# Optimization experiments

Measured on AMD Instinct MI355X. Metric: run time of the kernel, lower is better.

## Reference

```python
import jax, jax.numpy as jnp
import numpy as np

_Q_IN = 128          # Q7 fixed-point scale
_LUT_MIN = -1024     # covers exp(x) for x in [-8, 0]
_Q_OUT = 1 << 16     # Q16 output scale for exp LUT
_TOP_K = 2

# exp LUT: index i in [-1024, 0] -> int32(exp(i/128) * 2^16), matching _build_exp_lut
_EXP_LUT = (jnp.exp(jnp.arange(_LUT_MIN, 1, dtype=jnp.float32) / _Q_IN) * _Q_OUT).astype(jnp.int32)


def softmax_integer(logits):
    """Fixed-point INT32 softmax via Q16 exp LUT (drop-in for softmax)."""
    li = jnp.round(logits.astype(jnp.float32) * _Q_IN).astype(jnp.int32)
    shifted = jnp.clip(li - li.max(axis=-1, keepdims=True), _LUT_MIN, None)  # <= 0
    exp_vals = _EXP_LUT[shifted - _LUT_MIN]                                  # Q16 int32
    exp_sum = jnp.clip(exp_vals.sum(axis=-1, keepdims=True), 1, None)
    return exp_vals.astype(jnp.float32) / exp_sum.astype(jnp.float32)


def setup_inputs() -> dict:
    key = jax.random.key(0)
    k0, k1, k2, k3, k4 = jax.random.split(key, 5)
    B, S, H, I, E = 4, 2048, 2048, 5632, 8
    x = jax.random.normal(k0, (B, S, H), dtype=jnp.float32)
    w_gate = jax.random.normal(k1, (E, H), dtype=jnp.float32) * 0.02
    w1 = jax.random.normal(k2, (E, I, H), dtype=jnp.float32) * 0.02  # gate proj, [out,in]
    w2 = jax.random.normal(k3, (E, H, I), dtype=jnp.float32) * 0.02  # down proj
    w3 = jax.random.normal(k4, (E, I, H), dtype=jnp.float32) * 0.02  # up proj
    return {"x": x, "w_gate": w_gate, "w1": w1, "w2": w2, "w3": w3}


def reference(x, w_gate, w1, w2, w3):
    orig_shape = x.shape
    H = orig_shape[-1]
    xf = x.reshape(-1, H)                 # [T, H]
    T = xf.shape[0]
    E = w_gate.shape[0]

    router_logits = xf @ w_gate.T         # [T, E]
    routing_weights = softmax_integer(router_logits)
    top_w, top_i = jax.lax.top_k(routing_weights, _TOP_K)
    top_w = top_w / top_w.sum(axis=-1, keepdims=True)

    # dense per-(token, expert) combine weights; zero for unselected experts
    combine = jnp.zeros((T, E), xf.dtype).at[jnp.arange(T)[:, None], top_i].add(top_w)

    out = jnp.zeros_like(xf)
    for e in range(E):  # small fixed expert count
        h = jax.nn.silu(xf @ w1[e].T) * (xf @ w3[e].T)   # [T, I] SwiGLU
        out = out + combine[:, e:e + 1] * (h @ w2[e].T)  # weighted combine
    return out.reshape(orig_shape)
```

## Files before the change

kernel.cpp:

```cpp
#include <hip/hip_runtime.h>
#include <hip/hip_bf16.h>

#define T_TOK 8192
#define HD 2048
#define ID 5632
#define NE 8

typedef __bf16 bf16x8 __attribute__((ext_vector_type(8)));
typedef float f32x4 __attribute__((ext_vector_type(4)));

__global__ void k_build_lut(int* __restrict__ lut) {
    int i = blockIdx.x * blockDim.x + threadIdx.x;
    if (i <= 1024) {
        float xv = (float)(i - 1024) * (1.0f / 128.0f);
        lut[i] = (int)(expf(xv) * 65536.0f);
    }
}

__global__ __launch_bounds__(64)
void k_router(const float* __restrict__ x, const float* __restrict__ wg,
              const int* __restrict__ lut, int* __restrict__ counts,
              int* __restrict__ lists, float* __restrict__ wlist) {
    const int tok  = blockIdx.x;
    const int lane = threadIdx.x;
    const float* xr = x + (size_t)tok * HD;

    double dot[NE];
    #pragma unroll
    for (int e = 0; e < NE; ++e) {
        const float* wr = wg + e * HD;
        double acc = 0.0;
        for (int k = lane; k < HD; k += 64)
            acc += (double)xr[k] * (double)wr[k];
        #pragma unroll
        for (int off = 32; off > 0; off >>= 1)
            acc += __shfl_down(acc, off);
        dot[e] = acc;
    }
    if (lane == 0) {
        int li[NE];
        #pragma unroll
        for (int e = 0; e < NE; ++e)
            li[e] = (int)rintf((float)dot[e] * 128.0f);
        int m = li[0];
        #pragma unroll
        for (int e = 1; e < NE; ++e) m = li[e] > m ? li[e] : m;
        int ev[NE]; int s = 0;
        #pragma unroll
        for (int e = 0; e < NE; ++e) {
            int sh = li[e] - m;
            if (sh < -1024) sh = -1024;
            ev[e] = lut[sh + 1024];
            s += ev[e];
        }
        int i0 = 0;
        #pragma unroll
        for (int e = 1; e < NE; ++e) if (ev[e] > ev[i0]) i0 = e;
        int i1 = -1;
        #pragma unroll
        for (int e = 0; e < NE; ++e) {
            if (e == i0) continue;
            if (i1 < 0 || ev[e] > ev[i1]) i1 = e;
        }
        float fs = (float)s;
        float r0 = (float)ev[i0] / fs;
        float r1 = (float)ev[i1] / fs;
        float ts = r0 + r1;
        float w0 = r0 / ts, w1 = r1 / ts;

        int p0 = atomicAdd(&counts[i0], 1);
        lists[i0 * T_TOK + p0] = (tok << 1);
        wlist[i0 * T_TOK + p0] = w0;
        int p1 = atomicAdd(&counts[i1], 1);
        lists[i1 * T_TOK + p1] = (tok << 1) | 1;
        wlist[i1 * T_TOK + p1] = w1;
    }
}

__global__ __launch_bounds__(256)
void k_cvt_bf16(const float* __restrict__ src, __bf16* __restrict__ dst, long n8) {
    long i = (long)blockIdx.x * blockDim.x + threadIdx.x;
    const long stride = (long)gridDim.x * blockDim.x;
    for (; i < n8; i += stride) {
        const f32x4 v0 = *reinterpret_cast<const f32x4*>(src + i * 8);
        const f32x4 v1 = *reinterpret_cast<const f32x4*>(src + i * 8 + 4);
        bf16x8 h;
        h[0] = (__bf16)v0[0]; h[1] = (__bf16)v0[1]; h[2] = (__bf16)v0[2]; h[3] = (__bf16)v0[3];
        h[4] = (__bf16)v1[0]; h[5] = (__bf16)v1[1]; h[6] = (__bf16)v1[2]; h[7] = (__bf16)v1[3];
        *reinterpret_cast<bf16x8*>(dst + i * 8) = h;
    }
}

__device__ __forceinline__ void cvt_store8(void* lds_base, int woff, const float* __restrict__ src) {
    const f32x4 v0 = *reinterpret_cast<const f32x4*>(src);
    const f32x4 v1 = *reinterpret_cast<const f32x4*>(src + 4);
    bf16x8 h;
    h[0] = (__bf16)v0[0]; h[1] = (__bf16)v0[1]; h[2] = (__bf16)v0[2]; h[3] = (__bf16)v0[3];
    h[4] = (__bf16)v1[0]; h[5] = (__bf16)v1[1]; h[6] = (__bf16)v1[2]; h[7] = (__bf16)v1[3];
    *reinterpret_cast<bf16x8*>(reinterpret_cast<char*>(lds_base) + woff) = h;
}

__device__ __forceinline__ bf16x8 lds_frag(const void* lds_base, int row, int klo) {
    int off = (row * 128 + klo) ^ ((row & 7) << 4);
    return *reinterpret_cast<const bf16x8*>(reinterpret_cast<const char*>(lds_base) + off);
}

__device__ __forceinline__ void gload16(const void* g, void* l) {
    __builtin_amdgcn_global_load_lds(
        (const __attribute__((address_space(1))) unsigned int*)g,
        (__attribute__((address_space(3))) unsigned int*)l,
        16, 0, 0);
}


__global__ __launch_bounds__(512, 2)
void k_gateup_b16(const __bf16* __restrict__ xb, const __bf16* __restrict__ w1b,
                  const __bf16* __restrict__ w3b,
                  const int* __restrict__ counts, const int* __restrict__ lists,
                  __bf16* __restrict__ hbuf) {
    const int e   = blockIdx.z;
    const int cnt = counts[e];
    const int mt  = blockIdx.y;
    if (mt * 128 >= cnt) return;
    const int nt  = blockIdx.x;

    __shared__ __align__(16) __bf16 sX [2][8192];
    __shared__ __align__(16) __bf16 sW1[2][8192];
    __shared__ __align__(16) __bf16 sW3[2][8192];

    const int t    = threadIdx.x;
    const int lane = t & 63;
    const int wave = t >> 6;
    const int wm   = (wave >> 2) * 64;
    const int wn   = (wave & 3) * 32;

    const int lrow = lane >> 3;
    const int kel  = ((lane & 7) ^ lrow) * 8;

    const __bf16* gX[2]; const __bf16* g1[2]; const __bf16* g3[2];
    int ldo[2];
    #pragma unroll
    for (int cq = 0; cq < 2; ++cq) {
        const int c   = wave + cq * 8;
        const int row = c * 8 + lrow;
        int mi  = mt * 128 + row;
        int mic = mi < cnt - 1 ? mi : cnt - 1;
        int tok = lists[e * T_TOK + mic] >> 1;
        gX[cq] = xb + (size_t)tok * HD + kel;
        const int grow = nt * 128 + row;
        g1[cq] = w1b + ((size_t)e * ID + grow) * HD + kel;
        g3[cq] = w3b + ((size_t)e * ID + grow) * HD + kel;
        ldo[cq] = c * 1024;
    }

    f32x4 accg[4][2] = {};
    f32x4 accu[4][2] = {};

#define STAGE_A(b, kt) do { \
    _Pragma("unroll") \
    for (int cq = 0; cq < 2; ++cq) { \
        gload16(gX[cq] + (kt), (char*)sX [b] + ldo[cq]); \
        gload16(g1[cq] + (kt), (char*)sW1[b] + ldo[cq]); \
        gload16(g3[cq] + (kt), (char*)sW3[b] + ldo[cq]); \
    } } while (0)

#define COMPUTE_A(b) do { \
    const __bf16* bx = sX [b]; \
    const __bf16* b1 = sW1[b]; \
    const __bf16* b3 = sW3[b]; \
    __builtin_amdgcn_s_setprio(1); \
    _Pragma("unroll") \
    for (int kk = 0; kk < 2; ++kk) { \
        const int klo = kk * 64 + ((lane >> 4) << 4); \
        bf16x8 af[4], b1f[2], b3f[2]; \
        _Pragma("unroll") \
        for (int m = 0; m < 4; ++m) \
            af[m] = lds_frag(bx, wm + m * 16 + (lane & 15), klo); \
        _Pragma("unroll") \
        for (int n = 0; n < 2; ++n) { \
            int row = wn + n * 16 + (lane & 15); \
            b1f[n] = lds_frag(b1, row, klo); \
            b3f[n] = lds_frag(b3, row, klo); \
        } \
        _Pragma("unroll") \
        for (int m = 0; m < 4; ++m) \
            _Pragma("unroll") \
            for (int n = 0; n < 2; ++n) { \
                accg[m][n] = __builtin_amdgcn_mfma_f32_16x16x32_bf16(af[m], b1f[n], accg[m][n], 0, 0, 0); \
                accu[m][n] = __builtin_amdgcn_mfma_f32_16x16x32_bf16(af[m], b3f[n], accu[m][n], 0, 0, 0); \
            } \
    } \
    __builtin_amdgcn_s_setprio(0); \
    } while (0)

    const int NT = HD / 64;
    STAGE_A(0, 0);
    for (int it = 0; it < NT - 1; ++it) {
        STAGE_A((it + 1) & 1, (it + 1) * 64);
        asm volatile("s_waitcnt vmcnt(6)" ::: "memory");
        __builtin_amdgcn_s_barrier();
        COMPUTE_A(it & 1);
        __builtin_amdgcn_s_barrier();
    }
    asm volatile("s_waitcnt vmcnt(0)" ::: "memory");
    __builtin_amdgcn_s_barrier();
    COMPUTE_A((NT - 1) & 1);

    const int col_l = lane & 15;
    const int row_l = (lane >> 4) * 4;
    #pragma unroll
    for (int m = 0; m < 4; ++m) {
        #pragma unroll
        for (int j = 0; j < 4; ++j) {
            int tl = wm + m * 16 + row_l + j;
            int mi = mt * 128 + tl;
            if (mi < cnt) {
                int slot = lists[e * T_TOK + mi];
                __bf16* hrow = hbuf + (size_t)slot * ID + nt * 128 + wn;
                #pragma unroll
                for (int n = 0; n < 2; ++n) {
                    float g = accg[m][n][j];
                    float u = accu[m][n][j];
                    float hv = (g / (1.0f + expf(-g))) * u;
                    hrow[n * 16 + col_l] = (__bf16)hv;
                }
            }
        }
    }
#undef STAGE_A
#undef COMPUTE_A
}

__global__ __launch_bounds__(512, 2)
void k_down_b16(const __bf16* __restrict__ hbuf, const __bf16* __restrict__ w2b,
                const int* __restrict__ counts, const int* __restrict__ lists,
                const float* __restrict__ wlist, float* __restrict__ out) {
    const int e   = blockIdx.z;
    const int cnt = counts[e];
    const int mt  = blockIdx.y;
    if (mt * 128 >= cnt) return;
    const int nt  = blockIdx.x;

    __shared__ __align__(16) __bf16 sH[2][8192];
    __shared__ __align__(16) __bf16 sW[2][8192];

    const int t    = threadIdx.x;
    const int lane = t & 63;
    const int wave = t >> 6;
    const int wm   = (wave >> 2) * 64;
    const int wn   = (wave & 3) * 32;

    const int lrow = lane >> 3;
    const int kel  = ((lane & 7) ^ lrow) * 8;

    const __bf16* gH[2]; const __bf16* gW[2];
    int ldo[2];
    #pragma unroll
    for (int cq = 0; cq < 2; ++cq) {
        const int c   = wave + cq * 8;
        const int row = c * 8 + lrow;
        int mi  = mt * 128 + row;
        int mic = mi < cnt - 1 ? mi : cnt - 1;
        int slot = lists[e * T_TOK + mic];
        gH[cq] = hbuf + (size_t)slot * ID + kel;
        const int grow = nt * 128 + row;
        gW[cq] = w2b + ((size_t)e * HD + grow) * ID + kel;
        ldo[cq] = c * 1024;
    }

    f32x4 acc[4][2] = {};

#define STAGE_B(b, kt) do { \
    _Pragma("unroll") \
    for (int cq = 0; cq < 2; ++cq) { \
        gload16(gH[cq] + (kt), (char*)sH[b] + ldo[cq]); \
        gload16(gW[cq] + (kt), (char*)sW[b] + ldo[cq]); \
    } } while (0)

#define COMPUTE_B(b) do { \
    const __bf16* bh = sH[b]; \
    const __bf16* bw = sW[b]; \
    __builtin_amdgcn_s_setprio(1); \
    _Pragma("unroll") \
    for (int kk = 0; kk < 2; ++kk) { \
        const int klo = kk * 64 + ((lane >> 4) << 4); \
        bf16x8 af[4], bf[2]; \
        _Pragma("unroll") \
        for (int m = 0; m < 4; ++m) \
            af[m] = lds_frag(bh, wm + m * 16 + (lane & 15), klo); \
        _Pragma("unroll") \
        for (int n = 0; n < 2; ++n) \
            bf[n] = lds_frag(bw, wn + n * 16 + (lane & 15), klo); \
        _Pragma("unroll") \
        for (int m = 0; m < 4; ++m) \
            _Pragma("unroll") \
            for (int n = 0; n < 2; ++n) \
                acc[m][n] = __builtin_amdgcn_mfma_f32_16x16x32_bf16(af[m], bf[n], acc[m][n], 0, 0, 0); \
    } \
    __builtin_amdgcn_s_setprio(0); \
    } while (0)

    const int NT = ID / 64;
    STAGE_B(0, 0);
    for (int it = 0; it < NT - 1; ++it) {
        STAGE_B((it + 1) & 1, (it + 1) * 64);
        asm volatile("s_waitcnt vmcnt(4)" ::: "memory");
        __builtin_amdgcn_s_barrier();
        COMPUTE_B(it & 1);
        __builtin_amdgcn_s_barrier();
    }
    asm volatile("s_waitcnt vmcnt(0)" ::: "memory");
    __builtin_amdgcn_s_barrier();
    COMPUTE_B((NT - 1) & 1);

    const int col_l = lane & 15;
    const int row_l = (lane >> 4) * 4;
    #pragma unroll
    for (int m = 0; m < 4; ++m) {
        #pragma unroll
        for (int j = 0; j < 4; ++j) {
            int tl = wm + m * 16 + row_l + j;
            int mi = mt * 128 + tl;
            if (mi < cnt) {
                int slot = lists[e * T_TOK + mi];
                int tok  = slot >> 1;
                float w  = wlist[e * T_TOK + mi];
                float* orow = out + (size_t)tok * HD + nt * 128 + wn;
                #pragma unroll
                for (int n = 0; n < 2; ++n)
                    atomicAdd(&orow[n * 16 + col_l], w * acc[m][n][j]);
            }
        }
    }
#undef STAGE_B
#undef COMPUTE_B
}


__global__ __launch_bounds__(256)
void k_gateup_f32(const float* __restrict__ x, const float* __restrict__ w1,
                  const float* __restrict__ w3,
                  const int* __restrict__ counts, const int* __restrict__ lists,
                  __bf16* __restrict__ hbuf) {
    const int e   = blockIdx.z;
    const int cnt = counts[e];
    const int mt  = blockIdx.y;
    if (mt * 128 >= cnt) return;
    const int nt  = blockIdx.x;

    __shared__ __align__(16) __bf16 sX [128 * 64];
    __shared__ __align__(16) __bf16 sW1[128 * 64];
    __shared__ __align__(16) __bf16 sW3[128 * 64];

    const int t    = threadIdx.x;
    const int lane = t & 63;
    const int wave = t >> 6;
    const int wm   = (wave >> 1) * 64;
    const int wn   = (wave & 1) * 64;
    const int cc = t & 7;
    const int r0 = t >> 3;

    const float* srcX[4]; const float* src1[4]; const float* src3[4];
    int woff[4];
    #pragma unroll
    for (int q = 0; q < 4; ++q) {
        int row = r0 + 32 * q;
        int mi  = mt * 128 + row;
        int mic = mi < cnt - 1 ? mi : cnt - 1;
        int slot = lists[e * T_TOK + mic];
        int tok  = slot >> 1;
        srcX[q] = x + (size_t)tok * HD + cc * 8;
        int grow = nt * 128 + row;
        src1[q] = w1 + ((size_t)e * ID + grow) * HD + cc * 8;
        src3[q] = w3 + ((size_t)e * ID + grow) * HD + cc * 8;
        woff[q] = (row * 128 + cc * 16) ^ ((row & 7) << 4);
    }

    f32x4 accg[4][4] = {};
    f32x4 accu[4][4] = {};

    for (int kt = 0; kt < HD; kt += 64) {
        __syncthreads();
        #pragma unroll
        for (int q = 0; q < 4; ++q) {
            cvt_store8(sX,  srcX[q] ? woff[q] : 0, srcX[q] + kt);
            cvt_store8(sW1, woff[q], src1[q] + kt);
            cvt_store8(sW3, woff[q], src3[q] + kt);
        }
        __syncthreads();
        #pragma unroll
        for (int kk = 0; kk < 2; ++kk) {
            const int klo = kk * 64 + ((lane >> 4) << 4);
            bf16x8 af[4], b1f[4], b3f[4];
            #pragma unroll
            for (int m = 0; m < 4; ++m)
                af[m] = lds_frag(sX, wm + m * 16 + (lane & 15), klo);
            #pragma unroll
            for (int n = 0; n < 4; ++n) {
                int row = wn + n * 16 + (lane & 15);
                b1f[n] = lds_frag(sW1, row, klo);
                b3f[n] = lds_frag(sW3, row, klo);
            }
            #pragma unroll
            for (int m = 0; m < 4; ++m)
                #pragma unroll
                for (int n = 0; n < 4; ++n) {
                    accg[m][n] = __builtin_amdgcn_mfma_f32_16x16x32_bf16(af[m], b1f[n], accg[m][n], 0, 0, 0);
                    accu[m][n] = __builtin_amdgcn_mfma_f32_16x16x32_bf16(af[m], b3f[n], accu[m][n], 0, 0, 0);
                }
        }
    }

    const int col_l = lane & 15;
    const int row_l = (lane >> 4) * 4;
    #pragma unroll
    for (int m = 0; m < 4; ++m) {
        #pragma unroll
        for (int j = 0; j < 4; ++j) {
            int tl = wm + m * 16 + row_l + j;
            int mi = mt * 128 + tl;
            if (mi < cnt) {
                int slot = lists[e * T_TOK + mi];
                __bf16* hrow = hbuf + (size_t)slot * ID + nt * 128 + wn;
                #pragma unroll
                for (int n = 0; n < 4; ++n) {
                    float g = accg[m][n][j];
                    float u = accu[m][n][j];
                    float hv = (g / (1.0f + expf(-g))) * u;
                    hrow[n * 16 + col_l] = (__bf16)hv;
                }
            }
        }
    }
}

__global__ __launch_bounds__(256)
void k_down_f32(const __bf16* __restrict__ hbuf, const float* __restrict__ w2,
                const int* __restrict__ counts, const int* __restrict__ lists,
                const float* __restrict__ wlist, float* __restrict__ out) {
    const int e   = blockIdx.z;
    const int cnt = counts[e];
    const int mt  = blockIdx.y;
    if (mt * 128 >= cnt) return;
    const int nt  = blockIdx.x;

    __shared__ __align__(16) __bf16 sH[128 * 64];
    __shared__ __align__(16) __bf16 sW[128 * 64];

    const int t    = threadIdx.x;
    const int lane = t & 63;
    const int wave = t >> 6;
    const int wm   = (wave >> 1) * 64;
    const int wn   = (wave & 1) * 64;
    const int cc = t & 7;
    const int r0 = t >> 3;

    const __bf16* srcH[4]; const float* srcW[4];
    int woff[4];
    #pragma unroll
    for (int q = 0; q < 4; ++q) {
        int row = r0 + 32 * q;
        int mi  = mt * 128 + row;
        int mic = mi < cnt - 1 ? mi : cnt - 1;
        int slot = lists[e * T_TOK + mic];
        srcH[q] = hbuf + (size_t)slot * ID + cc * 8;
        int grow = nt * 128 + row;
        srcW[q] = w2 + ((size_t)e * HD + grow) * ID + cc * 8;
        woff[q] = (row * 128 + cc * 16) ^ ((row & 7) << 4);
    }

    f32x4 acc[4][4] = {};

    for (int kt = 0; kt < ID; kt += 64) {
        __syncthreads();
        #pragma unroll
        for (int q = 0; q < 4; ++q) {
            bf16x8 v = *reinterpret_cast<const bf16x8*>(srcH[q] + kt);
            *reinterpret_cast<bf16x8*>(reinterpret_cast<char*>(sH) + woff[q]) = v;
            cvt_store8(sW, woff[q], srcW[q] + kt);
        }
        __syncthreads();
        #pragma unroll
        for (int kk = 0; kk < 2; ++kk) {
            const int klo = kk * 64 + ((lane >> 4) << 4);
            bf16x8 af[4], bf[4];
            #pragma unroll
            for (int m = 0; m < 4; ++m)
                af[m] = lds_frag(sH, wm + m * 16 + (lane & 15), klo);
            #pragma unroll
            for (int n = 0; n < 4; ++n)
                bf[n] = lds_frag(sW, wn + n * 16 + (lane & 15), klo);
            #pragma unroll
            for (int m = 0; m < 4; ++m)
                #pragma unroll
                for (int n = 0; n < 4; ++n)
                    acc[m][n] = __builtin_amdgcn_mfma_f32_16x16x32_bf16(af[m], bf[n], acc[m][n], 0, 0, 0);
        }
    }

    const int col_l = lane & 15;
    const int row_l = (lane >> 4) * 4;
    #pragma unroll
    for (int m = 0; m < 4; ++m) {
        #pragma unroll
        for (int j = 0; j < 4; ++j) {
            int tl = wm + m * 16 + row_l + j;
            int mi = mt * 128 + tl;
            if (mi < cnt) {
                int slot = lists[e * T_TOK + mi];
                int tok  = slot >> 1;
                float w  = wlist[e * T_TOK + mi];
                float* orow = out + (size_t)tok * HD + nt * 128 + wn;
                #pragma unroll
                for (int n = 0; n < 4; ++n)
                    atomicAdd(&orow[n * 16 + col_l], w * acc[m][n][j]);
            }
        }
    }
}

extern "C" void kernel_launch(void* const* d_in, const int* in_sizes, int n_in,
                              void* d_out, int out_size, void* d_ws, size_t ws_size,
                              hipStream_t stream) {
    const float* x  = (const float*)d_in[0];
    const float* wg = (const float*)d_in[1];
    const float* w1 = (const float*)d_in[2];
    const float* w2 = (const float*)d_in[3];
    const float* w3 = (const float*)d_in[4];
    float* out = (float*)d_out;

    const size_t HBUF_B = (size_t)2 * T_TOK * ID * 2;
    const size_t XB_B   = (size_t)T_TOK * HD * 2;
    const size_t WB_B   = (size_t)NE * ID * HD * 2;
    const size_t SMALL  = 4608 + 512 + (size_t)NE * T_TOK * 4 * 2 + 4096;

    char* ws = (char*)d_ws;
    __bf16* hbuf = (__bf16*)ws;

    const size_t XB_OFF  = HBUF_B;
    const size_t W1_OFF  = XB_OFF + XB_B;
    const size_t W3_OFF  = W1_OFF + WB_B;
    const size_t W2_OFF  = W3_OFF + WB_B;
    const size_t TAIL    = W2_OFF + WB_B;
    const size_t NEED_FULL = TAIL + SMALL;
    const size_t NEED_MIN  = HBUF_B + SMALL;

    if (ws_size >= NEED_FULL) {
        __bf16* xb  = (__bf16*)(ws + XB_OFF);
        __bf16* w1b = (__bf16*)(ws + W1_OFF);
        __bf16* w3b = (__bf16*)(ws + W3_OFF);
        __bf16* w2b = (__bf16*)(ws + W2_OFF);
        int*   lut    = (int*)(ws + TAIL);
        int*   counts = (int*)(ws + TAIL + 4608);
        int*   lists  = (int*)(ws + TAIL + 4608 + 512);
        float* wlist  = (float*)(ws + TAIL + 4608 + 512 + (size_t)NE * T_TOK * 4);

        hipMemsetAsync(out, 0, (size_t)out_size * sizeof(float), stream);
        hipMemsetAsync(counts, 0, 64, stream);
        k_build_lut<<<dim3(5), dim3(256), 0, stream>>>(lut);
        k_router<<<dim3(T_TOK), dim3(64), 0, stream>>>(x, wg, lut, counts, lists, wlist);
        k_cvt_bf16<<<dim3(2048), dim3(256), 0, stream>>>(x,  xb,  (long)T_TOK * HD / 8);
        k_cvt_bf16<<<dim3(2048), dim3(256), 0, stream>>>(w1, w1b, (long)NE * ID * HD / 8);
        k_cvt_bf16<<<dim3(2048), dim3(256), 0, stream>>>(w3, w3b, (long)NE * ID * HD / 8);
        k_cvt_bf16<<<dim3(2048), dim3(256), 0, stream>>>(w2, w2b, (long)NE * ID * HD / 8);
        k_gateup_b16<<<dim3(ID / 128, T_TOK / 128, NE), dim3(512), 0, stream>>>(xb, w1b, w3b, counts, lists, hbuf);
        k_down_b16<<<dim3(HD / 128, T_TOK / 128, NE), dim3(512), 0, stream>>>(hbuf, w2b, counts, lists, wlist, out);
    } else if (ws_size >= NEED_MIN) {
        int*   lut    = (int*)(ws + HBUF_B);
        int*   counts = (int*)(ws + HBUF_B + 4608);
        int*   lists  = (int*)(ws + HBUF_B + 4608 + 512);
        float* wlist  = (float*)(ws + HBUF_B + 4608 + 512 + (size_t)NE * T_TOK * 4);

        hipMemsetAsync(out, 0, (size_t)out_size * sizeof(float), stream);
        hipMemsetAsync(counts, 0, 64, stream);
        k_build_lut<<<dim3(5), dim3(256), 0, stream>>>(lut);
        k_router<<<dim3(T_TOK), dim3(64), 0, stream>>>(x, wg, lut, counts, lists, wlist);
        k_gateup_f32<<<dim3(ID / 128, T_TOK / 128, NE), dim3(256), 0, stream>>>(x, w1, w3, counts, lists, hbuf);
        k_down_f32<<<dim3(HD / 128, T_TOK / 128, NE), dim3(256), 0, stream>>>(hbuf, w2, counts, lists, wlist, out);
    } else {
        hipMemsetAsync(d_out, 0x7F, (size_t)out_size * sizeof(float), stream);
    }
}
```

Before: 2.442 ms.

## Enlarge MoE GEMM tiles to 256-token blocks and reorder grid for weight reuse

```diff
diff --git a/kernel.cpp b/kernel.cpp
--- a/kernel.cpp
+++ b/kernel.cpp
@@ -25,13 +25,18 @@
     const int lane = threadIdx.x;
     const float* xr = x + (size_t)tok * HD;
 
+    float xc[32];
+    #pragma unroll
+    for (int kk = 0; kk < 32; ++kk) xc[kk] = xr[lane + kk * 64];
+
     double dot[NE];
     #pragma unroll
     for (int e = 0; e < NE; ++e) {
         const float* wr = wg + e * HD;
         double acc = 0.0;
-        for (int k = lane; k < HD; k += 64)
-            acc += (double)xr[k] * (double)wr[k];
+        #pragma unroll
+        for (int kk = 0; kk < 32; ++kk)
+            acc += (double)xc[kk] * (double)wr[lane + kk * 64];
         #pragma unroll
         for (int off = 32; off > 0; off >>= 1)
             acc += __shfl_down(acc, off);
@@ -113,71 +118,78 @@
 }
 
 
-__global__ __launch_bounds__(512, 2)
+__global__ __launch_bounds__(512)
 void k_gateup_b16(const __bf16* __restrict__ xb, const __bf16* __restrict__ w1b,
                   const __bf16* __restrict__ w3b,
                   const int* __restrict__ counts, const int* __restrict__ lists,
                   __bf16* __restrict__ hbuf) {
     const int e   = blockIdx.z;
     const int cnt = counts[e];
-    const int mt  = blockIdx.y;
-    if (mt * 128 >= cnt) return;
-    const int nt  = blockIdx.x;
-
-    __shared__ __align__(16) __bf16 sX [2][8192];
-    __shared__ __align__(16) __bf16 sW1[2][8192];
-    __shared__ __align__(16) __bf16 sW3[2][8192];
+    const int mt  = blockIdx.x;
+    if (mt * 256 >= cnt) return;
+    const int nt  = blockIdx.y;
+
+    __shared__ __align__(16) __bf16 sA [2][256 * 64];
+    __shared__ __align__(16) __bf16 sB1[2][128 * 64];
+    __shared__ __align__(16) __bf16 sB3[2][128 * 64];
 
     const int t    = threadIdx.x;
     const int lane = t & 63;
     const int wave = t >> 6;
-    const int wm   = (wave >> 2) * 64;
-    const int wn   = (wave & 3) * 32;
+    const int wm   = (wave >> 1) * 64;
+    const int wn   = (wave & 1) * 64;
 
     const int lrow = lane >> 3;
     const int kel  = ((lane & 7) ^ lrow) * 8;
 
-    const __bf16* gX[2]; const __bf16* g1[2]; const __bf16* g3[2];
-    int ldo[2];
-    #pragma unroll
-    for (int cq = 0; cq < 2; ++cq) {
-        const int c   = wave + cq * 8;
+    const __bf16* gA[4]; int loA[4];
+    #pragma unroll
+    for (int q = 0; q < 4; ++q) {
+        const int c   = wave + q * 8;
         const int row = c * 8 + lrow;
-        int mi  = mt * 128 + row;
+        int mi  = mt * 256 + row;
         int mic = mi < cnt - 1 ? mi : cnt - 1;
         int tok = lists[e * T_TOK + mic] >> 1;
-        gX[cq] = xb + (size_t)tok * HD + kel;
+        gA[q]  = xb + (size_t)tok * HD + kel;
+        loA[q] = c * 1024;
+    }
+    const __bf16* g1[2]; const __bf16* g3[2]; int loB[2];
+    #pragma unroll
+    for (int q = 0; q < 2; ++q) {
+        const int c   = wave + q * 8;
+        const int row = c * 8 + lrow;
         const int grow = nt * 128 + row;
-        g1[cq] = w1b + ((size_t)e * ID + grow) * HD + kel;
-        g3[cq] = w3b + ((size_t)e * ID + grow) * HD + kel;
-        ldo[cq] = c * 1024;
-    }
-
-    f32x4 accg[4][2] = {};
-    f32x4 accu[4][2] = {};
+        g1[q]  = w1b + ((size_t)e * ID + grow) * HD + kel;
+        g3[q]  = w3b + ((size_t)e * ID + grow) * HD + kel;
+        loB[q] = c * 1024;
+    }
+
+    f32x4 accg[4][4] = {};
+    f32x4 accu[4][4] = {};
 
 #define STAGE_A(b, kt) do { \
     _Pragma("unroll") \
-    for (int cq = 0; cq < 2; ++cq) { \
-        gload16(gX[cq] + (kt), (char*)sX [b] + ldo[cq]); \
-        gload16(g1[cq] + (kt), (char*)sW1[b] + ldo[cq]); \
-        gload16(g3[cq] + (kt), (char*)sW3[b] + ldo[cq]); \
+    for (int q = 0; q < 4; ++q) gload16(gA[q] + (kt), (char*)sA[b] + loA[q]); \
+    _Pragma("unroll") \
+    for (int q = 0; q < 2; ++q) { \
+        gload16(g1[q] + (kt), (char*)sB1[b] + loB[q]); \
+        gload16(g3[q] + (kt), (char*)sB3[b] + loB[q]); \
     } } while (0)
 
 #define COMPUTE_A(b) do { \
-    const __bf16* bx = sX [b]; \
-    const __bf16* b1 = sW1[b]; \
-    const __bf16* b3 = sW3[b]; \
+    const __bf16* ba = sA [b]; \
+    const __bf16* b1 = sB1[b]; \
+    const __bf16* b3 = sB3[b]; \
     __builtin_amdgcn_s_setprio(1); \
     _Pragma("unroll") \
     for (int kk = 0; kk < 2; ++kk) { \
         const int klo = kk * 64 + ((lane >> 4) << 4); \
-        bf16x8 af[4], b1f[2], b3f[2]; \
+        bf16x8 af[4], b1f[4], b3f[4]; \
         _Pragma("unroll") \
         for (int m = 0; m < 4; ++m) \
-            af[m] = lds_frag(bx, wm + m * 16 + (lane & 15), klo); \
+            af[m] = lds_frag(ba, wm + m * 16 + (lane & 15), klo); \
         _Pragma("unroll") \
-        for (int n = 0; n < 2; ++n) { \
+        for (int n = 0; n < 4; ++n) { \
             int row = wn + n * 16 + (lane & 15); \
             b1f[n] = lds_frag(b1, row, klo); \
             b3f[n] = lds_frag(b3, row, klo); \
@@ -185,7 +197,7 @@
         _Pragma("unroll") \
         for (int m = 0; m < 4; ++m) \
             _Pragma("unroll") \
-            for (int n = 0; n < 2; ++n) { \
+            for (int n = 0; n < 4; ++n) { \
                 accg[m][n] = __builtin_amdgcn_mfma_f32_16x16x32_bf16(af[m], b1f[n], accg[m][n], 0, 0, 0); \
                 accu[m][n] = __builtin_amdgcn_mfma_f32_16x16x32_bf16(af[m], b3f[n], accu[m][n], 0, 0, 0); \
             } \
@@ -197,7 +209,7 @@
     STAGE_A(0, 0);
     for (int it = 0; it < NT - 1; ++it) {
         STAGE_A((it + 1) & 1, (it + 1) * 64);
-        asm volatile("s_waitcnt vmcnt(6)" ::: "memory");
+        asm volatile("s_waitcnt vmcnt(8)" ::: "memory");
         __builtin_amdgcn_s_barrier();
         COMPUTE_A(it & 1);
         __builtin_amdgcn_s_barrier();
@@ -213,12 +225,12 @@
         #pragma unroll
         for (int j = 0; j < 4; ++j) {
             int tl = wm + m * 16 + row_l + j;
-            int mi = mt * 128 + tl;
+            int mi = mt * 256 + tl;
             if (mi < cnt) {
                 int slot = lists[e * T_TOK + mi];
                 __bf16* hrow = hbuf + (size_t)slot * ID + nt * 128 + wn;
                 #pragma unroll
-                for (int n = 0; n < 2; ++n) {
+                for (int n = 0; n < 4; ++n) {
                     float g = accg[m][n][j];
                     float u = accu[m][n][j];
                     float hv = (g / (1.0f + expf(-g))) * u;
@@ -231,50 +243,49 @@
 #undef COMPUTE_A
 }
 
-__global__ __launch_bounds__(512, 2)
+__global__ __launch_bounds__(512)
 void k_down_b16(const __bf16* __restrict__ hbuf, const __bf16* __restrict__ w2b,
                 const int* __restrict__ counts, const int* __restrict__ lists,
                 const float* __restrict__ wlist, float* __restrict__ out) {
     const int e   = blockIdx.z;
     const int cnt = counts[e];
-    const int mt  = blockIdx.y;
-    if (mt * 128 >= cnt) return;
-    const int nt  = blockIdx.x;
-
-    __shared__ __align__(16) __bf16 sH[2][8192];
-    __shared__ __align__(16) __bf16 sW[2][8192];
+    const int mt  = blockIdx.x;
+    if (mt * 256 >= cnt) return;
+    const int nt  = blockIdx.y;
+
+    __shared__ __align__(16) __bf16 sH[2][256 * 64];
+    __shared__ __align__(16) __bf16 sW[2][256 * 64];
 
     const int t    = threadIdx.x;
     const int lane = t & 63;
     const int wave = t >> 6;
-    const int wm   = (wave >> 2) * 64;
-    const int wn   = (wave & 3) * 32;
+    const int wm   = (wave >> 2) * 128;
+    const int wn   = (wave & 3) * 64;
 
     const int lrow = lane >> 3;
     const int kel  = ((lane & 7) ^ lrow) * 8;
 
-    const __bf16* gH[2]; const __bf16* gW[2];
-    int ldo[2];
-    #pragma unroll
-    for (int cq = 0; cq < 2; ++cq) {
-        const int c   = wave + cq * 8;
+    const __bf16* gH[4]; const __bf16* gW[4]; int loT[4];
+    #pragma unroll
+    for (int q = 0; q < 4; ++q) {
+        const int c   = wave + q * 8;
         const int row = c * 8 + lrow;
-        int mi  = mt * 128 + row;
+        int mi  = mt * 256 + row;
         int mic = mi < cnt - 1 ? mi : cnt - 1;
         int slot = lists[e * T_TOK + mic];
-        gH[cq] = hbuf + (size_t)slot * ID + kel;
-        const int grow = nt * 128 + row;
-        gW[cq] = w2b + ((size_t)e * HD + grow) * ID + kel;
-        ldo[cq] = c * 1024;
-    }
-
-    f32x4 acc[4][2] = {};
+        gH[q] = hbuf + (size_t)slot * ID + kel;
+        const int grow = nt * 256 + row;
+        gW[q] = w2b + ((size_t)e * HD + grow) * ID + kel;
+        loT[q] = c * 1024;
+    }
+
+    f32x4 acc[8][4] = {};
 
 #define STAGE_B(b, kt) do { \
     _Pragma("unroll") \
-    for (int cq = 0; cq < 2; ++cq) { \
-        gload16(gH[cq] + (kt), (char*)sH[b] + ldo[cq]); \
-        gload16(gW[cq] + (kt), (char*)sW[b] + ldo[cq]); \
+    for (int q = 0; q < 4; ++q) { \
+        gload16(gH[q] + (kt), (char*)sH[b] + loT[q]); \
+        gload16(gW[q] + (kt), (char*)sW[b] + loT[q]); \
     } } while (0)
 
 #define COMPUTE_B(b) do { \
@@ -284,17 +295,17 @@
     _Pragma("unroll") \
     for (int kk = 0; kk < 2; ++kk) { \
         const int klo = kk * 64 + ((lane >> 4) << 4); \
-        bf16x8 af[4], bf[2]; \
+        bf16x8 af[8], bf[4]; \
         _Pragma("unroll") \
-        for (int m = 0; m < 4; ++m) \
+        for (int m = 0; m < 8; ++m) \
             af[m] = lds_frag(bh, wm + m * 16 + (lane & 15), klo); \
         _Pragma("unroll") \
-        for (int n = 0; n < 2; ++n) \
+        for (int n = 0; n < 4; ++n) \
             bf[n] = lds_frag(bw, wn + n * 16 + (lane & 15), klo); \
         _Pragma("unroll") \
-        for (int m = 0; m < 4; ++m) \
+        for (int m = 0; m < 8; ++m) \
             _Pragma("unroll") \
-            for (int n = 0; n < 2; ++n) \
+            for (int n = 0; n < 4; ++n) \
                 acc[m][n] = __builtin_amdgcn_mfma_f32_16x16x32_bf16(af[m], bf[n], acc[m][n], 0, 0, 0); \
     } \
     __builtin_amdgcn_s_setprio(0); \
@@ -304,7 +315,7 @@
     STAGE_B(0, 0);
     for (int it = 0; it < NT - 1; ++it) {
         STAGE_B((it + 1) & 1, (it + 1) * 64);
-        asm volatile("s_waitcnt vmcnt(4)" ::: "memory");
+        asm volatile("s_waitcnt vmcnt(8)" ::: "memory");
         __builtin_amdgcn_s_barrier();
         COMPUTE_B(it & 1);
         __builtin_amdgcn_s_barrier();
@@ -316,18 +327,18 @@
     const int col_l = lane & 15;
     const int row_l = (lane >> 4) * 4;
     #pragma unroll
-    for (int m = 0; m < 4; ++m) {
+    for (int m = 0; m < 8; ++m) {
         #pragma unroll
         for (int j = 0; j < 4; ++j) {
             int tl = wm + m * 16 + row_l + j;
-            int mi = mt * 128 + tl;
+            int mi = mt * 256 + tl;
             if (mi < cnt) {
                 int slot = lists[e * T_TOK + mi];
                 int tok  = slot >> 1;
                 float w  = wlist[e * T_TOK + mi];
-                float* orow = out + (size_t)tok * HD + nt * 128 + wn;
+                float* orow = out + (size_t)tok * HD + nt * 256 + wn;
                 #pragma unroll
-                for (int n = 0; n < 2; ++n)
+                for (int n = 0; n < 4; ++n)
                     atomicAdd(&orow[n * 16 + col_l], w * acc[m][n][j]);
             }
         }
@@ -383,7 +394,7 @@
         __syncthreads();
         #pragma unroll
         for (int q = 0; q < 4; ++q) {
-            cvt_store8(sX,  srcX[q] ? woff[q] : 0, srcX[q] + kt);
+            cvt_store8(sX,  woff[q], srcX[q] + kt);
             cvt_store8(sW1, woff[q], src1[q] + kt);
             cvt_store8(sW3, woff[q], src3[q] + kt);
         }
@@ -555,29 +566,29 @@
         int*   lists  = (int*)(ws + TAIL + 4608 + 512);
         float* wlist  = (float*)(ws + TAIL + 4608 + 512 + (size_t)NE * T_TOK * 4);
 
-        hipMemsetAsync(out, 0, (size_t)out_size * sizeof(float), stream);
-        hipMemsetAsync(counts, 0, 64, stream);
+        (void)hipMemsetAsync(out, 0, (size_t)out_size * sizeof(float), stream);
+        (void)hipMemsetAsync(counts, 0, 64, stream);
         k_build_lut<<<dim3(5), dim3(256), 0, stream>>>(lut);
         k_router<<<dim3(T_TOK), dim3(64), 0, stream>>>(x, wg, lut, counts, lists, wlist);
         k_cvt_bf16<<<dim3(2048), dim3(256), 0, stream>>>(x,  xb,  (long)T_TOK * HD / 8);
         k_cvt_bf16<<<dim3(2048), dim3(256), 0, stream>>>(w1, w1b, (long)NE * ID * HD / 8);
         k_cvt_bf16<<<dim3(2048), dim3(256), 0, stream>>>(w3, w3b, (long)NE * ID * HD / 8);
         k_cvt_bf16<<<dim3(2048), dim3(256), 0, stream>>>(w2, w2b, (long)NE * ID * HD / 8);
-        k_gateup_b16<<<dim3(ID / 128, T_TOK / 128, NE), dim3(512), 0, stream>>>(xb, w1b, w3b, counts, lists, hbuf);
-        k_down_b16<<<dim3(HD / 128, T_TOK / 128, NE), dim3(512), 0, stream>>>(hbuf, w2b, counts, lists, wlist, out);
+        k_gateup_b16<<<dim3(T_TOK / 256, ID / 128, NE), dim3(512), 0, stream>>>(xb, w1b, w3b, counts, lists, hbuf);
+        k_down_b16<<<dim3(T_TOK / 256, HD / 256, NE), dim3(512), 0, stream>>>(hbuf, w2b, counts, lists, wlist, out);
     } else if (ws_size >= NEED_MIN) {
         int*   lut    = (int*)(ws + HBUF_B);
         int*   counts = (int*)(ws + HBUF_B + 4608);
         int*   lists  = (int*)(ws + HBUF_B + 4608 + 512);
         float* wlist  = (float*)(ws + HBUF_B + 4608 + 512 + (size_t)NE * T_TOK * 4);
 
-        hipMemsetAsync(out, 0, (size_t)out_size * sizeof(float), stream);
-        hipMemsetAsync(counts, 0, 64, stream);
+        (void)hipMemsetAsync(out, 0, (size_t)out_size * sizeof(float), stream);
+        (void)hipMemsetAsync(counts, 0, 64, stream);
         k_build_lut<<<dim3(5), dim3(256), 0, stream>>>(lut);
         k_router<<<dim3(T_TOK), dim3(64), 0, stream>>>(x, wg, lut, counts, lists, wlist);
         k_gateup_f32<<<dim3(ID / 128, T_TOK / 128, NE), dim3(256), 0, stream>>>(x, w1, w3, counts, lists, hbuf);
         k_down_f32<<<dim3(HD / 128, T_TOK / 128, NE), dim3(256), 0, stream>>>(hbuf, w2, counts, lists, wlist, out);
     } else {
-        hipMemsetAsync(d_out, 0x7F, (size_t)out_size * sizeof(float), stream);
-    }
-}
+        (void)hipMemsetAsync(d_out, 0x7F, (size_t)out_size * sizeof(float), stream);
+    }
+}
```

After: 5.463 ms. +123.7%, slower.
